# Performance work log

Hardware: AMD Instinct MI355X
Metric: run time of the kernel (lower is better)

The kernel has to match this reference:

```python
import jax, jax.numpy as jnp
import numpy as np

NB_HEADS = 4
EMBED_DIM = 128
EPS = 1e-06


def setup_inputs() -> dict:
    key = jax.random.key(0)
    ks = jax.random.split(key, 9)
    B, R, C, E = 2, 64, 2048, 128
    s = 1.0 / np.sqrt(E)
    inp = {
        "input": jax.random.normal(ks[0], (B, R, C, E), dtype=jnp.float32),
        # weights stored as (in, out); torch Linear applies x @ W.T + b, equivalent here
        "Wq": jax.random.normal(ks[1], (E, E), dtype=jnp.float32) * s,
        "bq": jax.random.normal(ks[2], (E,), dtype=jnp.float32) * 0.01,
        "Wk": jax.random.normal(ks[3], (E, E), dtype=jnp.float32) * s,
        "bk": jax.random.normal(ks[4], (E,), dtype=jnp.float32) * 0.01,
        "Wv": jax.random.normal(ks[5], (E, E), dtype=jnp.float32) * s,
        "bv": jax.random.normal(ks[6], (E,), dtype=jnp.float32) * 0.01,
        "Wo": jax.random.normal(ks[7], (E, E), dtype=jnp.float32) * s,
        "bo": jax.random.normal(ks[8], (E,), dtype=jnp.float32) * 0.01,
    }
    return inp


def reference(input, Wq, bq, Wk, bk, Wv, bv, Wo, bo):
    B, R, C, E = input.shape
    H = NB_HEADS
    Dh = E // H
    # projections, split into heads: (B, R, C, H, Dh)
    q = (input @ Wq + bq).reshape(B, R, C, H, Dh)
    k = (input @ Wk + bk).reshape(B, R, C, H, Dh)
    v = (input @ Wv + bv).reshape(B, R, C, H, Dh)
    # elu+1 feature map
    q = jax.nn.elu(q) + 1.0
    k = jax.nn.elu(k) + 1.0
    # KtV: contract over col axis -> (B, R, H, Dh, Dh)
    KtV = jnp.einsum('brchd,brche->brhde', k, v)
    # normalizer: q . sum_c(k) -> (B, R, C, H)
    ksum = k.sum(axis=2)  # (B, R, H, Dh)
    Z = 1.0 / (jnp.einsum('brchd,brhd->brch', q, ksum) + EPS)
    # attention output: (B, R, C, H, Dh)
    out = jnp.einsum('brchd,brhde->brche', q, KtV) * Z[..., None]
    out = out.reshape(B, R, C, E)
    return out @ Wo + bo
```

## Files before the change

kernel.cpp:

```cpp
#include <hip/hip_runtime.h>

#define DEVINL __device__ __forceinline__

typedef __attribute__((ext_vector_type(8))) __bf16 bf16x8;
typedef __attribute__((ext_vector_type(4))) __bf16 bf16x4;
typedef __attribute__((ext_vector_type(4))) float f32x4;

DEVINL f32x4 mfma16(bf16x8 a, bf16x8 b, f32x4 c) {
  return __builtin_amdgcn_mfma_f32_16x16x32_bf16(a, b, c, 0, 0, 0);
}

DEVINL bf16x8 loadWfrag(const float* __restrict__ W, int kb, int n) {
  bf16x8 f;
#pragma unroll
  for (int j = 0; j < 8; ++j) f[j] = (__bf16)W[(kb + j) * 128 + n];
  return f;
}

__global__ __launch_bounds__(256, 2)
void qkv_ktv_kernel(const float* __restrict__ X,
                    const float* __restrict__ Wq, const float* __restrict__ bq,
                    const float* __restrict__ Wk, const float* __restrict__ bk,
                    const float* __restrict__ Wv, const float* __restrict__ bv,
                    __bf16* __restrict__ Qout,
                    float* __restrict__ ktvWs, float* __restrict__ ksumWs)
{
  __shared__ __bf16 Xs[64 * 136];
  __shared__ __bf16 Kt[128 * 72];
  __shared__ __bf16 Vt[128 * 72];

  const int tid  = threadIdx.x;
  const int lane = tid & 63;
  const int w    = tid >> 6;
  const int l15  = lane & 15;
  const int quad = lane >> 4;
  const int s     = blockIdx.x >> 2;
  const int chunk = blockIdx.x & 3;
  const int tokc0 = chunk * 512;
  const float* Xseq = X + (size_t)s * 2048 * 128;

  bf16x8 wkF[2][4], wvF[2][4], wqF[2][4];
#pragma unroll
  for (int nt = 0; nt < 2; ++nt) {
    const int n = w * 32 + nt * 16 + l15;
#pragma unroll
    for (int kk = 0; kk < 4; ++kk) {
      const int kb = kk * 32 + quad * 8;
      wkF[nt][kk] = loadWfrag(Wk, kb, n);
      wvF[nt][kk] = loadWfrag(Wv, kb, n);
      wqF[nt][kk] = loadWfrag(Wq, kb, n);
    }
  }
  float bkr[2], bvr[2], bqr[2][4];
#pragma unroll
  for (int nt = 0; nt < 2; ++nt) {
    bkr[nt] = bk[w * 32 + nt * 16 + l15];
    bvr[nt] = bv[w * 32 + nt * 16 + l15];
#pragma unroll
    for (int r = 0; r < 4; ++r)
      bqr[nt][r] = bq[w * 32 + nt * 16 + quad * 4 + r];
  }

  f32x4 accT[2][2] = {};
  float ksumAcc[2] = {0.f, 0.f};

  for (int t = 0; t < 8; ++t) {
    const float* Xtile = Xseq + (size_t)(tokc0 + t * 64) * 128;
    __syncthreads();
#pragma unroll
    for (int i = 0; i < 8; ++i) {
      const int flat = tid + i * 256;
      const int row = flat >> 5;
      const int c4  = (flat & 31) * 4;
      const float4 v = *(const float4*)(Xtile + row * 128 + c4);
      bf16x4 b4;
      b4[0] = (__bf16)v.x; b4[1] = (__bf16)v.y;
      b4[2] = (__bf16)v.z; b4[3] = (__bf16)v.w;
      *(bf16x4*)(&Xs[row * 136 + c4]) = b4;
    }
    __syncthreads();

#pragma unroll
    for (int mt = 0; mt < 4; ++mt) {
      f32x4 aK[2] = {}, aV[2] = {};
#pragma unroll
      for (int kk = 0; kk < 4; ++kk) {
        const bf16x8 ax = *(const bf16x8*)(&Xs[(mt * 16 + l15) * 136 + kk * 32 + quad * 8]);
        aK[0] = mfma16(ax, wkF[0][kk], aK[0]);
        aK[1] = mfma16(ax, wkF[1][kk], aK[1]);
        aV[0] = mfma16(ax, wvF[0][kk], aV[0]);
        aV[1] = mfma16(ax, wvF[1][kk], aV[1]);
      }
#pragma unroll
      for (int nt = 0; nt < 2; ++nt) {
        const int e    = w * 32 + nt * 16 + l15;
        const int tokb = mt * 16 + quad * 4;
        bf16x4 kq, vq;
        float ks = 0.f;
#pragma unroll
        for (int r = 0; r < 4; ++r) {
          float kv = aK[nt][r] + bkr[nt];
          kv = (kv > 0.f) ? (kv + 1.f) : __expf(kv);
          ks += kv;
          kq[r] = (__bf16)kv;
          vq[r] = (__bf16)(aV[nt][r] + bvr[nt]);
        }
        ksumAcc[nt] += ks;
        *(bf16x4*)(&Kt[e * 72 + tokb]) = kq;
        *(bf16x4*)(&Vt[e * 72 + tokb]) = vq;
      }
    }

#pragma unroll
    for (int ntq = 0; ntq < 4; ++ntq) {
      f32x4 aQ[2] = {};
#pragma unroll
      for (int kk = 0; kk < 4; ++kk) {
        const bf16x8 bx = *(const bf16x8*)(&Xs[(ntq * 16 + l15) * 136 + kk * 32 + quad * 8]);
        aQ[0] = mfma16(wqF[0][kk], bx, aQ[0]);
        aQ[1] = mfma16(wqF[1][kk], bx, aQ[1]);
      }
      const int tok = tokc0 + t * 64 + ntq * 16 + l15;
      __bf16* qrow = Qout + ((size_t)s * 2048 + tok) * 128;
#pragma unroll
      for (int mt = 0; mt < 2; ++mt) {
        bf16x4 qq;
#pragma unroll
        for (int r = 0; r < 4; ++r) {
          float qv = aQ[mt][r] + bqr[mt][r];
          qv = (qv > 0.f) ? (qv + 1.f) : __expf(qv);
          qq[r] = (__bf16)qv;
        }
        *(bf16x4*)(qrow + w * 32 + mt * 16 + quad * 4) = qq;
      }
    }
    __syncthreads();

#pragma unroll
    for (int kk = 0; kk < 2; ++kk) {
      bf16x8 aF[2], bF[2];
#pragma unroll
      for (int dt = 0; dt < 2; ++dt)
        aF[dt] = *(const bf16x8*)(&Kt[(w * 32 + dt * 16 + l15) * 72 + kk * 32 + quad * 8]);
#pragma unroll
      for (int et = 0; et < 2; ++et)
        bF[et] = *(const bf16x8*)(&Vt[(w * 32 + et * 16 + l15) * 72 + kk * 32 + quad * 8]);
#pragma unroll
      for (int dt = 0; dt < 2; ++dt)
#pragma unroll
        for (int et = 0; et < 2; ++et)
          accT[dt][et] = mfma16(aF[dt], bF[et], accT[dt][et]);
    }
  }

  float* ktvH = ktvWs + ((size_t)s * 4 + w) * 1024;
#pragma unroll
  for (int dt = 0; dt < 2; ++dt)
#pragma unroll
    for (int et = 0; et < 2; ++et)
#pragma unroll
      for (int r = 0; r < 4; ++r)
        atomicAdd(&ktvH[(dt * 16 + quad * 4 + r) * 32 + et * 16 + l15], accT[dt][et][r]);

#pragma unroll
  for (int nt = 0; nt < 2; ++nt) {
    float v2 = ksumAcc[nt];
    v2 += __shfl_down(v2, 32);
    v2 += __shfl_down(v2, 16);
    if (quad == 0)
      atomicAdd(&ksumWs[s * 128 + w * 32 + nt * 16 + l15], v2);
  }
}

__global__ __launch_bounds__(256, 2)
void attn_out_kernel(const __bf16* __restrict__ Qin,
                     const float* __restrict__ ktvWs, const float* __restrict__ ksumWs,
                     const float* __restrict__ Wo, const float* __restrict__ bo,
                     float* __restrict__ Out)
{
  __shared__ __bf16 Qs[64 * 136];
  __shared__ __bf16 A2s[64 * 136];
  __shared__ float ksums[128];
  __shared__ float Zs[64 * 4];

  const int tid  = threadIdx.x;
  const int lane = tid & 63;
  const int w    = tid >> 6;
  const int l15  = lane & 15;
  const int quad = lane >> 4;
  const int s     = blockIdx.x >> 2;
  const int chunk = blockIdx.x & 3;

  if (tid < 128) ksums[tid] = ksumWs[s * 128 + tid];

  const float* ktvH = ktvWs + ((size_t)s * 4 + w) * 1024;
  bf16x8 aKtv[2];
#pragma unroll
  for (int mt = 0; mt < 2; ++mt)
#pragma unroll
    for (int j = 0; j < 8; ++j)
      aKtv[mt][j] = (__bf16)ktvH[(quad * 8 + j) * 32 + mt * 16 + l15];

  bf16x8 woF[2][4];
  float bor[2];
#pragma unroll
  for (int nt = 0; nt < 2; ++nt) {
    const int n = w * 32 + nt * 16 + l15;
    bor[nt] = bo[n];
#pragma unroll
    for (int kk = 0; kk < 4; ++kk)
      woF[nt][kk] = loadWfrag(Wo, kk * 32 + quad * 8, n);
  }
  __syncthreads();

  for (int t = 0; t < 8; ++t) {
    const int tok0 = chunk * 512 + t * 64;
    const __bf16* Qtile = Qin + ((size_t)s * 2048 + tok0) * 128;
    __syncthreads();
#pragma unroll
    for (int i = 0; i < 4; ++i) {
      const int c = tid + i * 256;
      const int row = c >> 4, cc = (c & 15) * 8;
      *(bf16x8*)(&Qs[row * 136 + cc]) = *(const bf16x8*)(Qtile + row * 128 + cc);
    }
    __syncthreads();
    {
      const int tok = tid >> 2, h = tid & 3;
      float dot = 0.f;
      const __bf16* qrow = &Qs[tok * 136 + h * 32];
      const float* ksrow = &ksums[h * 32];
#pragma unroll
      for (int j = 0; j < 32; ++j) dot += (float)qrow[j] * ksrow[j];
      Zs[tok * 4 + h] = 1.f / (dot + 1e-6f);
    }
    __syncthreads();
#pragma unroll
    for (int ntq = 0; ntq < 4; ++ntq) {
      const bf16x8 bq8 = *(const bf16x8*)(&Qs[(ntq * 16 + l15) * 136 + w * 32 + quad * 8]);
      f32x4 acc[2] = {};
      acc[0] = mfma16(aKtv[0], bq8, acc[0]);
      acc[1] = mfma16(aKtv[1], bq8, acc[1]);
      const int tokRow = ntq * 16 + l15;
      const float z = Zs[tokRow * 4 + w];
#pragma unroll
      for (int mt = 0; mt < 2; ++mt) {
        bf16x4 a4;
#pragma unroll
        for (int r = 0; r < 4; ++r) a4[r] = (__bf16)(acc[mt][r] * z);
        *(bf16x4*)(&A2s[tokRow * 136 + w * 32 + mt * 16 + quad * 4]) = a4;
      }
    }
    __syncthreads();
#pragma unroll
    for (int mt = 0; mt < 4; ++mt) {
      f32x4 acc[2] = {};
#pragma unroll
      for (int kk = 0; kk < 4; ++kk) {
        const bf16x8 aa = *(const bf16x8*)(&A2s[(mt * 16 + l15) * 136 + kk * 32 + quad * 8]);
        acc[0] = mfma16(aa, woF[0][kk], acc[0]);
        acc[1] = mfma16(aa, woF[1][kk], acc[1]);
      }
      const int tokb = tok0 + mt * 16 + quad * 4;
      float* orow = Out + ((size_t)s * 2048 + tokb) * 128;
#pragma unroll
      for (int nt = 0; nt < 2; ++nt) {
        const int n = w * 32 + nt * 16 + l15;
#pragma unroll
        for (int r = 0; r < 4; ++r)
          orow[(size_t)r * 128 + n] = acc[nt][r] + bor[nt];
      }
    }
  }
}

extern "C" void kernel_launch(void* const* d_in, const int* in_sizes, int n_in,
                              void* d_out, int out_size, void* d_ws, size_t ws_size,
                              hipStream_t stream) {
  const float* X  = (const float*)d_in[0];
  const float* Wq = (const float*)d_in[1];
  const float* bq = (const float*)d_in[2];
  const float* Wk = (const float*)d_in[3];
  const float* bk = (const float*)d_in[4];
  const float* Wv = (const float*)d_in[5];
  const float* bv = (const float*)d_in[6];
  const float* Wo = (const float*)d_in[7];
  const float* bo = (const float*)d_in[8];
  float* Out = (float*)d_out;

  const size_t Q_BYTES    = (size_t)128 * 2048 * 128 * 2;
  const size_t KTV_BYTES  = (size_t)128 * 4 * 32 * 32 * 4;
  const size_t KSUM_BYTES = (size_t)128 * 128 * 4;
  __bf16* Qws   = (__bf16*)d_ws;
  float* ktvWs  = (float*)((char*)d_ws + Q_BYTES);
  float* ksumWs = (float*)((char*)d_ws + Q_BYTES + KTV_BYTES);

  hipMemsetAsync((char*)d_ws + Q_BYTES, 0, KTV_BYTES + KSUM_BYTES, stream);

  qkv_ktv_kernel<<<dim3(512), dim3(256), 0, stream>>>(
      X, Wq, bq, Wk, bk, Wv, bv, Qws, ktvWs, ksumWs);
  attn_out_kernel<<<dim3(512), dim3(256), 0, stream>>>(
      Qws, ktvWs, ksumWs, Wo, bo, Out);
}
```

Measured before the change: 310.5 us.

## Prefetch input tiles into registers, drop barriers, and rework output kernel grid

In the projection kernel, the next X tile is loaded into registers while the current tile is processed. The KtV MFMA is moved before the Q projection, which lets one barrier per iteration be removed. In the output kernel, the grid doubles to 1024 blocks with 256 tokens each and the occupancy hint goes from 2 to 4. The normalizer is now computed in registers with shuffles instead of a separate shared-memory pass with extra barriers. The output projection is transposed so each thread writes float4 stores. These changes aim to hide global load latency, cut synchronization, and coalesce output writes, at the cost of higher register pressure.

```diff
diff --git a/kernel.cpp b/kernel.cpp
--- a/kernel.cpp
+++ b/kernel.cpp
@@ -39,6 +39,16 @@
   const int tokc0 = chunk * 512;
   const float* Xseq = X + (size_t)s * 2048 * 128;
 
+  float4 xst[8];
+  {
+    const float* Xt0 = Xseq + (size_t)tokc0 * 128;
+#pragma unroll
+    for (int i = 0; i < 8; ++i) {
+      const int flat = tid + i * 256;
+      xst[i] = *(const float4*)(Xt0 + (flat >> 5) * 128 + (flat & 31) * 4);
+    }
+  }
+
   bf16x8 wkF[2][4], wvF[2][4], wqF[2][4];
 #pragma unroll
   for (int nt = 0; nt < 2; ++nt) {
@@ -65,18 +75,24 @@
   float ksumAcc[2] = {0.f, 0.f};
 
   for (int t = 0; t < 8; ++t) {
-    const float* Xtile = Xseq + (size_t)(tokc0 + t * 64) * 128;
     __syncthreads();
 #pragma unroll
     for (int i = 0; i < 8; ++i) {
       const int flat = tid + i * 256;
       const int row = flat >> 5;
       const int c4  = (flat & 31) * 4;
-      const float4 v = *(const float4*)(Xtile + row * 128 + c4);
       bf16x4 b4;
-      b4[0] = (__bf16)v.x; b4[1] = (__bf16)v.y;
-      b4[2] = (__bf16)v.z; b4[3] = (__bf16)v.w;
+      b4[0] = (__bf16)xst[i].x; b4[1] = (__bf16)xst[i].y;
+      b4[2] = (__bf16)xst[i].z; b4[3] = (__bf16)xst[i].w;
       *(bf16x4*)(&Xs[row * 136 + c4]) = b4;
+    }
+    if (t < 7) {
+      const float* Xn = Xseq + (size_t)(tokc0 + (t + 1) * 64) * 128;
+#pragma unroll
+      for (int i = 0; i < 8; ++i) {
+        const int flat = tid + i * 256;
+        xst[i] = *(const float4*)(Xn + (flat >> 5) * 128 + (flat & 31) * 4);
+      }
     }
     __syncthreads();
 
@@ -112,6 +128,22 @@
     }
 
 #pragma unroll
+    for (int kk = 0; kk < 2; ++kk) {
+      bf16x8 aF[2], bF[2];
+#pragma unroll
+      for (int dt = 0; dt < 2; ++dt)
+        aF[dt] = *(const bf16x8*)(&Kt[(w * 32 + dt * 16 + l15) * 72 + kk * 32 + quad * 8]);
+#pragma unroll
+      for (int et = 0; et < 2; ++et)
+        bF[et] = *(const bf16x8*)(&Vt[(w * 32 + et * 16 + l15) * 72 + kk * 32 + quad * 8]);
+#pragma unroll
+      for (int dt = 0; dt < 2; ++dt)
+#pragma unroll
+        for (int et = 0; et < 2; ++et)
+          accT[dt][et] = mfma16(aF[dt], bF[et], accT[dt][et]);
+    }
+
+#pragma unroll
     for (int ntq = 0; ntq < 4; ++ntq) {
       f32x4 aQ[2] = {};
 #pragma unroll
@@ -134,23 +166,6 @@
         *(bf16x4*)(qrow + w * 32 + mt * 16 + quad * 4) = qq;
       }
     }
-    __syncthreads();
-
-#pragma unroll
-    for (int kk = 0; kk < 2; ++kk) {
-      bf16x8 aF[2], bF[2];
-#pragma unroll
-      for (int dt = 0; dt < 2; ++dt)
-        aF[dt] = *(const bf16x8*)(&Kt[(w * 32 + dt * 16 + l15) * 72 + kk * 32 + quad * 8]);
-#pragma unroll
-      for (int et = 0; et < 2; ++et)
-        bF[et] = *(const bf16x8*)(&Vt[(w * 32 + et * 16 + l15) * 72 + kk * 32 + quad * 8]);
-#pragma unroll
-      for (int dt = 0; dt < 2; ++dt)
-#pragma unroll
-        for (int et = 0; et < 2; ++et)
-          accT[dt][et] = mfma16(aF[dt], bF[et], accT[dt][et]);
-    }
   }
 
   float* ktvH = ktvWs + ((size_t)s * 4 + w) * 1024;
@@ -172,7 +187,7 @@
   }
 }
 
-__global__ __launch_bounds__(256, 2)
+__global__ __launch_bounds__(256, 4)
 void attn_out_kernel(const __bf16* __restrict__ Qin,
                      const float* __restrict__ ktvWs, const float* __restrict__ ksumWs,
                      const float* __restrict__ Wo, const float* __restrict__ bo,
@@ -180,18 +195,22 @@
 {
   __shared__ __bf16 Qs[64 * 136];
   __shared__ __bf16 A2s[64 * 136];
-  __shared__ float ksums[128];
-  __shared__ float Zs[64 * 4];
 
   const int tid  = threadIdx.x;
   const int lane = tid & 63;
   const int w    = tid >> 6;
   const int l15  = lane & 15;
   const int quad = lane >> 4;
-  const int s     = blockIdx.x >> 2;
-  const int chunk = blockIdx.x & 3;
-
-  if (tid < 128) ksums[tid] = ksumWs[s * 128 + tid];
+  const int s     = blockIdx.x >> 3;
+  const int chunk = blockIdx.x & 7;
+  const __bf16* Qc = Qin + ((size_t)s * 2048 + chunk * 256) * 128;
+
+  bf16x8 qst[4];
+#pragma unroll
+  for (int i = 0; i < 4; ++i) {
+    const int c = tid + i * 256;
+    qst[i] = *(const bf16x8*)(Qc + (c >> 4) * 128 + (c & 15) * 8);
+  }
 
   const float* ktvH = ktvWs + ((size_t)s * 4 + w) * 1024;
   bf16x8 aKtv[2];
@@ -201,73 +220,83 @@
     for (int j = 0; j < 8; ++j)
       aKtv[mt][j] = (__bf16)ktvH[(quad * 8 + j) * 32 + mt * 16 + l15];
 
+  float ksum8[8];
+#pragma unroll
+  for (int j = 0; j < 8; ++j)
+    ksum8[j] = ksumWs[s * 128 + w * 32 + quad * 8 + j];
+
   bf16x8 woF[2][4];
-  float bor[2];
+  float borr[2][4];
 #pragma unroll
   for (int nt = 0; nt < 2; ++nt) {
     const int n = w * 32 + nt * 16 + l15;
-    bor[nt] = bo[n];
 #pragma unroll
     for (int kk = 0; kk < 4; ++kk)
       woF[nt][kk] = loadWfrag(Wo, kk * 32 + quad * 8, n);
-  }
-  __syncthreads();
-
-  for (int t = 0; t < 8; ++t) {
-    const int tok0 = chunk * 512 + t * 64;
-    const __bf16* Qtile = Qin + ((size_t)s * 2048 + tok0) * 128;
+#pragma unroll
+    for (int r = 0; r < 4; ++r)
+      borr[nt][r] = bo[w * 32 + nt * 16 + quad * 4 + r];
+  }
+
+  for (int t = 0; t < 4; ++t) {
+    const int tok0 = chunk * 256 + t * 64;
     __syncthreads();
 #pragma unroll
     for (int i = 0; i < 4; ++i) {
       const int c = tid + i * 256;
-      const int row = c >> 4, cc = (c & 15) * 8;
-      *(bf16x8*)(&Qs[row * 136 + cc]) = *(const bf16x8*)(Qtile + row * 128 + cc);
-    }
-    __syncthreads();
-    {
-      const int tok = tid >> 2, h = tid & 3;
-      float dot = 0.f;
-      const __bf16* qrow = &Qs[tok * 136 + h * 32];
-      const float* ksrow = &ksums[h * 32];
-#pragma unroll
-      for (int j = 0; j < 32; ++j) dot += (float)qrow[j] * ksrow[j];
-      Zs[tok * 4 + h] = 1.f / (dot + 1e-6f);
-    }
-    __syncthreads();
+      *(bf16x8*)(&Qs[(c >> 4) * 136 + (c & 15) * 8]) = qst[i];
+    }
+    if (t < 3) {
+      const __bf16* Qn = Qc + (size_t)(t + 1) * 64 * 128;
+#pragma unroll
+      for (int i = 0; i < 4; ++i) {
+        const int c = tid + i * 256;
+        qst[i] = *(const bf16x8*)(Qn + (c >> 4) * 128 + (c & 15) * 8);
+      }
+    }
+    __syncthreads();
+
 #pragma unroll
     for (int ntq = 0; ntq < 4; ++ntq) {
       const bf16x8 bq8 = *(const bf16x8*)(&Qs[(ntq * 16 + l15) * 136 + w * 32 + quad * 8]);
+      float dot = 0.f;
+#pragma unroll
+      for (int j = 0; j < 8; ++j) dot += (float)bq8[j] * ksum8[j];
+      dot += __shfl_xor(dot, 16);
+      dot += __shfl_xor(dot, 32);
+      const float z = 1.f / (dot + 1e-6f);
       f32x4 acc[2] = {};
       acc[0] = mfma16(aKtv[0], bq8, acc[0]);
       acc[1] = mfma16(aKtv[1], bq8, acc[1]);
-      const int tokRow = ntq * 16 + l15;
-      const float z = Zs[tokRow * 4 + w];
 #pragma unroll
       for (int mt = 0; mt < 2; ++mt) {
         bf16x4 a4;
 #pragma unroll
         for (int r = 0; r < 4; ++r) a4[r] = (__bf16)(acc[mt][r] * z);
-        *(bf16x4*)(&A2s[tokRow * 136 + w * 32 + mt * 16 + quad * 4]) = a4;
-      }
-    }
-    __syncthreads();
-#pragma unroll
-    for (int mt = 0; mt < 4; ++mt) {
+        *(bf16x4*)(&A2s[(ntq * 16 + l15) * 136 + w * 32 + mt * 16 + quad * 4]) = a4;
+      }
+    }
+    __syncthreads();
+
+#pragma unroll
+    for (int ntq = 0; ntq < 4; ++ntq) {
       f32x4 acc[2] = {};
 #pragma unroll
       for (int kk = 0; kk < 4; ++kk) {
-        const bf16x8 aa = *(const bf16x8*)(&A2s[(mt * 16 + l15) * 136 + kk * 32 + quad * 8]);
-        acc[0] = mfma16(aa, woF[0][kk], acc[0]);
-        acc[1] = mfma16(aa, woF[1][kk], acc[1]);
-      }
-      const int tokb = tok0 + mt * 16 + quad * 4;
-      float* orow = Out + ((size_t)s * 2048 + tokb) * 128;
+        const bf16x8 a2f = *(const bf16x8*)(&A2s[(ntq * 16 + l15) * 136 + kk * 32 + quad * 8]);
+        acc[0] = mfma16(woF[0][kk], a2f, acc[0]);
+        acc[1] = mfma16(woF[1][kk], a2f, acc[1]);
+      }
+      const int tok = tok0 + ntq * 16 + l15;
+      float* orow = Out + ((size_t)s * 2048 + tok) * 128;
 #pragma unroll
       for (int nt = 0; nt < 2; ++nt) {
-        const int n = w * 32 + nt * 16 + l15;
-#pragma unroll
-        for (int r = 0; r < 4; ++r)
-          orow[(size_t)r * 128 + n] = acc[nt][r] + bor[nt];
+        float4 o4;
+        o4.x = acc[nt][0] + borr[nt][0];
+        o4.y = acc[nt][1] + borr[nt][1];
+        o4.z = acc[nt][2] + borr[nt][2];
+        o4.w = acc[nt][3] + borr[nt][3];
+        *(float4*)(orow + w * 32 + nt * 16 + quad * 4) = o4;
       }
     }
   }
@@ -298,6 +327,6 @@
 
   qkv_ktv_kernel<<<dim3(512), dim3(256), 0, stream>>>(
       X, Wq, bq, Wk, bk, Wv, bv, Qws, ktvWs, ksumWs);
-  attn_out_kernel<<<dim3(512), dim3(256), 0, stream>>>(
+  attn_out_kernel<<<dim3(1024), dim3(256), 0, stream>>>(
       Qws, ktvWs, ksumWs, Wo, bo, Out);
 }
```

After: 310.5 us. No clear change (+0.0%).
